# Kernel tuning notes

Measured on AMD Instinct MI355X. Metric: run time of the kernel, lower is better.

## Reference

```python
import jax, jax.numpy as jnp
import numpy as np

N_NODES = 20000
N_EDGES = 640000
C_IN = 128      # num_node_features
K_FOLDS = 8     # num_edge_features
FILTERS = 128


def setup_inputs() -> dict:
    key = jax.random.key(0)
    k1, k2, k3, k4, k5, k6 = jax.random.split(key, 6)
    node_features = jax.random.normal(k1, (N_NODES, C_IN), dtype=jnp.float32)
    edge_features = jax.random.uniform(k2, (K_FOLDS, N_EDGES), dtype=jnp.float32)
    rows = jax.random.randint(k3, (N_EDGES,), 0, N_NODES)
    cols = jax.random.randint(k4, (N_EDGES,), 0, N_NODES)
    indices = jnp.stack([rows, cols], axis=1).astype(jnp.int64)
    # glorot_uniform kernel [K, C_in, filters]
    limit = np.sqrt(6.0 / (C_IN + FILTERS))
    kernel = jax.random.uniform(k5, (K_FOLDS, C_IN, FILTERS), dtype=jnp.float32,
                                minval=-limit, maxval=limit)
    bias = jnp.zeros((FILTERS,), dtype=jnp.float32)
    return {
        "node_features": node_features,
        "edge_features": edge_features,
        "kernel": kernel,
        "bias": bias,
        "indices": indices,
        "out_size": N_NODES,
    }


def reference(node_features, edge_features, kernel, bias, indices, out_size):
    # fold_conv: out[i,f] = sum_{e: row(e)=i} sum_k ef[k,e] * (x[col(e)] @ kernel[k])[f]
    row = indices[:, 0]
    col = indices[:, 1]
    xg = node_features[col]  # [E, C] gathered source-node features
    E = xg.shape[0]
    msgs = jnp.zeros((E, kernel.shape[2]), dtype=node_features.dtype)
    # Loop over the small fixed number of folds (K=8); each iteration is a
    # dense [E,C]x[C,F] matmul scaled by the per-edge fold weight.
    for k in range(kernel.shape[0]):
        msgs = msgs + (xg @ kernel[k]) * edge_features[k][:, None]
    out = jax.ops.segment_sum(msgs, row, num_segments=out_size)  # [out_size, F]
    out = out + bias  # bias_add; activation is None (linear)
    return out
```

## Files before the change

kernel.cpp:

```cpp
#include <hip/hip_runtime.h>
#include <cstddef>
#include <cstdint>

static constexpr int kNodes   = 20000;
static constexpr int kEdges   = 640000;
static constexpr int kCin     = 128;
static constexpr int kFolds   = 8;
static constexpr int kFilters = 128;
static constexpr int kKdim    = kFolds * kCin;
static constexpr int kCap     = 80;

static constexpr int kNBucket = 250;
static constexpr int kRowsPB  = 80;
static constexpr int kCapB    = 3072;
static constexpr int kBin1Blk = 160;

typedef __attribute__((ext_vector_type(8))) short v8s;
typedef __attribute__((ext_vector_type(4))) float v4f;

__device__ __forceinline__ unsigned short f2bf(float f) {
    union { float f; uint32_t u; } v; v.f = f;
    const uint32_t u = v.u;
    return (unsigned short)((u + 0x7fffu + ((u >> 16) & 1u)) >> 16);
}
__device__ __forceinline__ float bf2f(unsigned short s) {
    union { uint32_t u; float f; } v; v.u = ((uint32_t)s) << 16;
    return v.f;
}

__global__ __launch_bounds__(256) void prep_k(
    const int2*  __restrict__ idx2,
    const float* __restrict__ ef,
    const float* __restrict__ x,
    const float* __restrict__ W,
    int* __restrict__ bucketCnt,
    int2* __restrict__ pairs,
    unsigned int* __restrict__ rec,
    unsigned short* __restrict__ xb,
    unsigned short* __restrict__ Wt)
{
    const int b = blockIdx.x;
    const int t = threadIdx.x;
    if (b < 2500) {
        const int e = b * 256 + t;
        const int2 rc = idx2[e];
        union { uint4 q; unsigned int w[4]; unsigned short s[8]; } o;
        #pragma unroll
        for (int k = 0; k < kFolds; ++k)
            o.s[k] = f2bf(ef[(size_t)k * kEdges + e]);
        uint4* recp = (uint4*)(rec + (size_t)e * 8);
        recp[0] = make_uint4((unsigned)rc.y, o.w[0], o.w[1], o.w[2]);
        recp[1] = make_uint4(o.w[3], 0u, 0u, 0u);
    } else if (b < 3750) {
        const int i = (b - 2500) * 2048 + t * 8;
        const float4 a = *(const float4*)(x + i);
        const float4 c = *(const float4*)(x + i + 4);
        union { uint4 q; unsigned short s[8]; } o;
        o.s[0] = f2bf(a.x); o.s[1] = f2bf(a.y); o.s[2] = f2bf(a.z); o.s[3] = f2bf(a.w);
        o.s[4] = f2bf(c.x); o.s[5] = f2bf(c.y); o.s[6] = f2bf(c.z); o.s[7] = f2bf(c.w);
        *(uint4*)(xb + i) = o.q;
    } else if (b < 3814) {
        const int t2 = (b - 3750) * 256 + t;
        const int n  = t2 & 127;
        const int k8 = t2 >> 7;
        union { uint4 q; unsigned short s[8]; } o;
        #pragma unroll
        for (int j = 0; j < 8; ++j)
            o.s[j] = f2bf(W[(size_t)(k8 * 8 + j) * kFilters + n]);
        *(uint4*)(Wt + (size_t)n * kKdim + k8 * 8) = o.q;
    } else {
        __shared__ int hist[kNBucket];
        __shared__ int base[kNBucket];
        const int bb = b - 3814;
        const int e0 = bb * 4096;

        if (t < kNBucket) hist[t] = 0;
        __syncthreads();

        int rowsReg[16];
        #pragma unroll
        for (int i = 0; i < 16; ++i) {
            const int e = e0 + i * 256 + t;
            int row = -1;
            if (e < kEdges) {
                row = idx2[e].x;
                atomicAdd(&hist[row / kRowsPB], 1);
            }
            rowsReg[i] = row;
        }
        __syncthreads();

        if (t < kNBucket) {
            const int h = hist[t];
            base[t] = atomicAdd(&bucketCnt[t], h);
            hist[t] = 0;
        }
        __syncthreads();

        #pragma unroll
        for (int i = 0; i < 16; ++i) {
            const int row = rowsReg[i];
            if (row >= 0) {
                const int e  = e0 + i * 256 + t;
                const int bk = row / kRowsPB;
                const int sl = base[bk] + atomicAdd(&hist[bk], 1);
                if (sl < kCapB)
                    pairs[(size_t)bk * kCapB + sl] = make_int2(row, e);
            }
        }
    }
}

__global__ __launch_bounds__(256) void bin2_k(
    const int2* __restrict__ pairs,
    const int*  __restrict__ bucketCnt,
    int* __restrict__ ebuf,
    int* __restrict__ cnt)
{
    __shared__ int c80[kRowsPB];
    const int b = blockIdx.x;
    const int t = threadIdx.x;

    if (t < kRowsPB) c80[t] = 0;
    __syncthreads();

    int n = bucketCnt[b];
    n = n < kCapB ? n : kCapB;
    const int2* seg = pairs + (size_t)b * kCapB;

    for (int s = t; s < n; s += 256) {
        const int2 p = seg[s];
        const int rl = p.x - b * kRowsPB;
        const int c  = atomicAdd(&c80[rl], 1);
        if (c < kCap) ebuf[p.x * kCap + c] = p.y;
    }
    __syncthreads();

    if (t < kRowsPB) cnt[b * kRowsPB + t] = c80[t];
}

__global__ __launch_bounds__(256) void pull_k(
    const unsigned short* __restrict__ xb,
    const int*  __restrict__ ebuf,
    const unsigned int* __restrict__ rec,
    const int*  __restrict__ cnt,
    unsigned short* __restrict__ S)
{
    __shared__ int   sCol[16][kCap + 4];
    __shared__ float sEf[16][kCap + 4][8];
    __shared__ int   sDeg[16];

    const int t  = threadIdx.x;
    const int n0 = blockIdx.x * 16;

    {
        const int g16 = t >> 4;
        const int s0  = t & 15;
        const int nn  = n0 + g16;
        int dg = cnt[nn];
        dg = dg < kCap ? dg : kCap;
        for (int s = s0; s < dg; s += 16) {
            const int e = ebuf[nn * kCap + s];
            const uint4 q0    = *(const uint4*)(rec + (size_t)e * 8);
            const unsigned w3 = rec[(size_t)e * 8 + 4];
            sCol[g16][s] = (int)q0.x;
            sEf[g16][s][0] = bf2f((unsigned short)(q0.y));
            sEf[g16][s][1] = bf2f((unsigned short)(q0.y >> 16));
            sEf[g16][s][2] = bf2f((unsigned short)(q0.z));
            sEf[g16][s][3] = bf2f((unsigned short)(q0.z >> 16));
            sEf[g16][s][4] = bf2f((unsigned short)(q0.w));
            sEf[g16][s][5] = bf2f((unsigned short)(q0.w >> 16));
            sEf[g16][s][6] = bf2f((unsigned short)(w3));
            sEf[g16][s][7] = bf2f((unsigned short)(w3 >> 16));
        }
        const int dgP = (dg + 3) & ~3;
        for (int s = dg + s0; s < dgP; s += 16) {
            sCol[g16][s] = 0;
            #pragma unroll
            for (int k = 0; k < kFolds; ++k) sEf[g16][s][k] = 0.f;
        }
        if (s0 == 0) sDeg[g16] = dg;
    }
    __syncthreads();

    const int wave = t >> 6;
    const int lane = t & 63;
    const int g    = lane >> 4;
    const int c8   = (lane & 15) * 8;
    const int ln   = wave * 4 + g;
    const int node = n0 + ln;
    const int degP = (sDeg[ln] + 3) & ~3;

    float acc[8][8];
    #pragma unroll
    for (int k = 0; k < 8; ++k)
        #pragma unroll
        for (int j = 0; j < 8; ++j) acc[k][j] = 0.f;

    const unsigned short* xbase = xb + c8;

    auto proc = [&](v8s xv, int i) {
        float xf[8];
        #pragma unroll
        for (int jj = 0; jj < 8; ++jj) xf[jj] = bf2f((unsigned short)xv[jj]);
        const float4 wa = *(const float4*)&sEf[ln][i][0];
        const float4 wc = *(const float4*)&sEf[ln][i][4];
        const float w[8] = {wa.x, wa.y, wa.z, wa.w, wc.x, wc.y, wc.z, wc.w};
        #pragma unroll
        for (int k = 0; k < 8; ++k)
            #pragma unroll
            for (int jj = 0; jj < 8; ++jj)
                acc[k][jj] += w[k] * xf[jj];
    };

    v8s x0 = (v8s)0, x1 = (v8s)0, x2 = (v8s)0, x3 = (v8s)0;
    if (degP > 0) {
        x0 = *(const v8s*)(xbase + (size_t)sCol[ln][0] * kCin);
        x1 = *(const v8s*)(xbase + (size_t)sCol[ln][1] * kCin);
        x2 = *(const v8s*)(xbase + (size_t)sCol[ln][2] * kCin);
        x3 = *(const v8s*)(xbase + (size_t)sCol[ln][3] * kCin);
    }

    for (int i = 0; i < degP; i += 4) {
        const int j = (i + 4 < degP) ? (i + 4) : i;
        const v8s y0 = *(const v8s*)(xbase + (size_t)sCol[ln][j]     * kCin);
        const v8s y1 = *(const v8s*)(xbase + (size_t)sCol[ln][j + 1] * kCin);
        const v8s y2 = *(const v8s*)(xbase + (size_t)sCol[ln][j + 2] * kCin);
        const v8s y3 = *(const v8s*)(xbase + (size_t)sCol[ln][j + 3] * kCin);

        proc(x0, i); proc(x1, i + 1); proc(x2, i + 2); proc(x3, i + 3);

        x0 = y0; x1 = y1; x2 = y2; x3 = y3;
    }

    unsigned short* srow = S + (size_t)node * kKdim + c8;
    #pragma unroll
    for (int k = 0; k < 8; ++k) {
        union { uint4 q; unsigned short s[8]; } o;
        #pragma unroll
        for (int j = 0; j < 8; ++j) o.s[j] = f2bf(acc[k][j]);
        *(uint4*)(srow + k * kCin) = o.q;
    }
}

static constexpr int BM  = 64;
static constexpr int BK  = 64;
static constexpr int SWS = 72;

__global__ __launch_bounds__(256) void gemm_k(
    const unsigned short* __restrict__ S,
    const unsigned short* __restrict__ Wt,
    const float* __restrict__ bias,
    float* __restrict__ out)
{
    __shared__ unsigned short sS[BM * SWS];
    __shared__ unsigned short sWt[kFilters * SWS];

    const int t    = threadIdx.x;
    const int wave = t >> 6;
    const int lane = t & 63;
    const int quad = lane >> 4;
    const int r16  = lane & 15;
    const int m0   = blockIdx.x * BM;

    v4f acc[8];
    #pragma unroll
    for (int i = 0; i < 8; ++i) acc[i] = (v4f){0.f, 0.f, 0.f, 0.f};

    for (int k0 = 0; k0 < kKdim; k0 += BK) {
        {
            const int row = t >> 2;
            const int kc  = (t & 3) * 16;
            const int m   = m0 + row;
            uint4 v0 = make_uint4(0, 0, 0, 0), v1 = make_uint4(0, 0, 0, 0);
            if (m < kNodes) {
                const unsigned short* src = S + (size_t)m * kKdim + k0 + kc;
                v0 = *(const uint4*)(src);
                v1 = *(const uint4*)(src + 8);
            }
            *(uint4*)&sS[row * SWS + kc]     = v0;
            *(uint4*)&sS[row * SWS + kc + 8] = v1;
        }
        {
            const int n    = t >> 1;
            const int half = (t & 1) * 32;
            const unsigned short* src = Wt + (size_t)n * kKdim + k0 + half;
            *(uint4*)&sWt[n * SWS + half]      = *(const uint4*)(src);
            *(uint4*)&sWt[n * SWS + half + 8]  = *(const uint4*)(src + 8);
            *(uint4*)&sWt[n * SWS + half + 16] = *(const uint4*)(src + 16);
            *(uint4*)&sWt[n * SWS + half + 24] = *(const uint4*)(src + 24);
        }
        __syncthreads();

        #pragma unroll
        for (int kk = 0; kk < 2; ++kk) {
            const v8s a = *(const v8s*)&sS[(wave * 16 + r16) * SWS + kk * 32 + quad * 8];
            #pragma unroll
            for (int nt = 0; nt < 8; ++nt) {
                const v8s b = *(const v8s*)&sWt[(nt * 16 + r16) * SWS + kk * 32 + quad * 8];
                acc[nt] = __builtin_amdgcn_mfma_f32_16x16x32_bf16(a, b, acc[nt], 0, 0, 0);
            }
        }
        __syncthreads();
    }

    #pragma unroll
    for (int nt = 0; nt < 8; ++nt) {
        const int n = nt * 16 + r16;
        const float bv = bias[n];
        #pragma unroll
        for (int r = 0; r < 4; ++r) {
            const int m = m0 + wave * 16 + quad * 4 + r;
            if (m < kNodes)
                out[(size_t)m * kFilters + n] = acc[nt][r] + bv;
        }
    }
}

extern "C" void kernel_launch(void* const* d_in, const int* in_sizes, int n_in,
                              void* d_out, int out_size, void* d_ws, size_t ws_size,
                              hipStream_t stream) {
    const float* x    = (const float*)d_in[0];
    const float* ef   = (const float*)d_in[1];
    const float* W    = (const float*)d_in[2];
    const float* bias = (const float*)d_in[3];
    const int2*  idx2 = (const int2*)d_in[4];
    float* out = (float*)d_out;

    char* ws = (char*)d_ws;
    unsigned short* S      = (unsigned short*)(ws);
    int2*           pairs  = (int2*)(ws);
    unsigned int*   rec    = (unsigned int*)(ws + 40960000);
    int*            ebuf   = (int*)(ws + 61440000);
    unsigned short* xb     = (unsigned short*)(ws + 67840000);
    unsigned short* Wt     = (unsigned short*)(ws + 72960000);
    int*            cnt    = (int*)(ws + 73222144);
    int*            bucketCnt = (int*)(ws + 73302144);

    hipMemsetAsync(bucketCnt, 0, kNBucket * sizeof(int), stream);

    prep_k<<<3814 + kBin1Blk, 256, 0, stream>>>(idx2, ef, x, W, bucketCnt,
                                                pairs, rec, xb, Wt);
    bin2_k<<<kNBucket, 256, 0, stream>>>(pairs, bucketCnt, ebuf, cnt);
    pull_k<<<kNodes / 16, 256, 0, stream>>>(xb, ebuf, rec, cnt, S);
    gemm_k<<<(kNodes + BM - 1) / BM, 256, 0, stream>>>(S, Wt, bias, out);
}
```

Measured before the change: 183.6 us.

## Fuse the GEMM into the pull kernel, dropping the S intermediate buffer

After: 192.0 us. 1.05x slower.

```diff
diff --git a/kernel.cpp b/kernel.cpp
--- a/kernel.cpp
+++ b/kernel.cpp
@@ -139,16 +139,23 @@
     if (t < kRowsPB) cnt[b * kRowsPB + t] = c80[t];
 }
 
+static constexpr int kSWS2 = 1048;
+
 __global__ __launch_bounds__(256) void pull_k(
     const unsigned short* __restrict__ xb,
     const int*  __restrict__ ebuf,
     const unsigned int* __restrict__ rec,
     const int*  __restrict__ cnt,
-    unsigned short* __restrict__ S)
+    const unsigned short* __restrict__ Wt,
+    const float* __restrict__ bias,
+    float* __restrict__ out)
 {
-    __shared__ int   sCol[16][kCap + 4];
-    __shared__ float sEf[16][kCap + 4][8];
-    __shared__ int   sDeg[16];
+    __shared__ int sCol[16][kCap + 4];
+    __shared__ int sDeg[16];
+    __shared__ __align__(16) char arena[16 * (kCap + 4) * 8 * 4];
+
+    float (*sEf)[kCap + 4][8] = (float(*)[kCap + 4][8])arena;
+    unsigned short (*sS)[kSWS2] = (unsigned short(*)[kSWS2])arena;
 
     const int t  = threadIdx.x;
     const int n0 = blockIdx.x * 16;
@@ -188,7 +195,6 @@
     const int g    = lane >> 4;
     const int c8   = (lane & 15) * 8;
     const int ln   = wave * 4 + g;
-    const int node = n0 + ln;
     const int degP = (sDeg[ln] + 3) & ~3;
 
     float acc[8][8];
@@ -233,86 +239,43 @@
         x0 = y0; x1 = y1; x2 = y2; x3 = y3;
     }
 
-    unsigned short* srow = S + (size_t)node * kKdim + c8;
+    __syncthreads();
     #pragma unroll
     for (int k = 0; k < 8; ++k) {
         union { uint4 q; unsigned short s[8]; } o;
         #pragma unroll
         for (int j = 0; j < 8; ++j) o.s[j] = f2bf(acc[k][j]);
-        *(uint4*)(srow + k * kCin) = o.q;
-    }
-}
-
-static constexpr int BM  = 64;
-static constexpr int BK  = 64;
-static constexpr int SWS = 72;
-
-__global__ __launch_bounds__(256) void gemm_k(
-    const unsigned short* __restrict__ S,
-    const unsigned short* __restrict__ Wt,
-    const float* __restrict__ bias,
-    float* __restrict__ out)
-{
-    __shared__ unsigned short sS[BM * SWS];
-    __shared__ unsigned short sWt[kFilters * SWS];
-
-    const int t    = threadIdx.x;
-    const int wave = t >> 6;
-    const int lane = t & 63;
+        *(uint4*)&sS[ln][k * kCin + c8] = o.q;
+    }
+    __syncthreads();
+
     const int quad = lane >> 4;
     const int r16  = lane & 15;
-    const int m0   = blockIdx.x * BM;
-
-    v4f acc[8];
+
+    v4f acc2[2];
+    acc2[0] = (v4f){0.f, 0.f, 0.f, 0.f};
+    acc2[1] = (v4f){0.f, 0.f, 0.f, 0.f};
+
+    const unsigned short* wt0 = Wt + (size_t)(wave * 32 + r16) * kKdim;
+    const unsigned short* wt1 = wt0 + (size_t)16 * kKdim;
+
+    #pragma unroll 4
+    for (int kc = 0; kc < kKdim; kc += 32) {
+        const v8s a  = *(const v8s*)&sS[r16][kc + quad * 8];
+        const v8s b0 = *(const v8s*)(wt0 + kc + quad * 8);
+        const v8s b1 = *(const v8s*)(wt1 + kc + quad * 8);
+        acc2[0] = __builtin_amdgcn_mfma_f32_16x16x32_bf16(a, b0, acc2[0], 0, 0, 0);
+        acc2[1] = __builtin_amdgcn_mfma_f32_16x16x32_bf16(a, b1, acc2[1], 0, 0, 0);
+    }
+
     #pragma unroll
-    for (int i = 0; i < 8; ++i) acc[i] = (v4f){0.f, 0.f, 0.f, 0.f};
-
-    for (int k0 = 0; k0 < kKdim; k0 += BK) {
-        {
-            const int row = t >> 2;
-            const int kc  = (t & 3) * 16;
-            const int m   = m0 + row;
-            uint4 v0 = make_uint4(0, 0, 0, 0), v1 = make_uint4(0, 0, 0, 0);
-            if (m < kNodes) {
-                const unsigned short* src = S + (size_t)m * kKdim + k0 + kc;
-                v0 = *(const uint4*)(src);
-                v1 = *(const uint4*)(src + 8);
-            }
-            *(uint4*)&sS[row * SWS + kc]     = v0;
-            *(uint4*)&sS[row * SWS + kc + 8] = v1;
-        }
-        {
-            const int n    = t >> 1;
-            const int half = (t & 1) * 32;
-            const unsigned short* src = Wt + (size_t)n * kKdim + k0 + half;
-            *(uint4*)&sWt[n * SWS + half]      = *(const uint4*)(src);
-            *(uint4*)&sWt[n * SWS + half + 8]  = *(const uint4*)(src + 8);
-            *(uint4*)&sWt[n * SWS + half + 16] = *(const uint4*)(src + 16);
-            *(uint4*)&sWt[n * SWS + half + 24] = *(const uint4*)(src + 24);
-        }
-        __syncthreads();
-
-        #pragma unroll
-        for (int kk = 0; kk < 2; ++kk) {
-            const v8s a = *(const v8s*)&sS[(wave * 16 + r16) * SWS + kk * 32 + quad * 8];
-            #pragma unroll
-            for (int nt = 0; nt < 8; ++nt) {
-                const v8s b = *(const v8s*)&sWt[(nt * 16 + r16) * SWS + kk * 32 + quad * 8];
-                acc[nt] = __builtin_amdgcn_mfma_f32_16x16x32_bf16(a, b, acc[nt], 0, 0, 0);
-            }
-        }
-        __syncthreads();
-    }
-
-    #pragma unroll
-    for (int nt = 0; nt < 8; ++nt) {
-        const int n = nt * 16 + r16;
+    for (int i = 0; i < 2; ++i) {
+        const int n  = (wave * 2 + i) * 16 + r16;
         const float bv = bias[n];
         #pragma unroll
         for (int r = 0; r < 4; ++r) {
-            const int m = m0 + wave * 16 + quad * 4 + r;
-            if (m < kNodes)
-                out[(size_t)m * kFilters + n] = acc[nt][r] + bv;
+            const int m = n0 + quad * 4 + r;
+            out[(size_t)m * kFilters + n] = acc2[i][r] + bv;
         }
     }
 }
@@ -328,7 +291,6 @@
     float* out = (float*)d_out;
 
     char* ws = (char*)d_ws;
-    unsigned short* S      = (unsigned short*)(ws);
     int2*           pairs  = (int2*)(ws);
     unsigned int*   rec    = (unsigned int*)(ws + 40960000);
     int*            ebuf   = (int*)(ws + 61440000);
@@ -342,6 +304,5 @@
     prep_k<<<3814 + kBin1Blk, 256, 0, stream>>>(idx2, ef, x, W, bucketCnt,
                                                 pairs, rec, xb, Wt);
     bin2_k<<<kNBucket, 256, 0, stream>>>(pairs, bucketCnt, ebuf, cnt);
-    pull_k<<<kNodes / 16, 256, 0, stream>>>(xb, ebuf, rec, cnt, S);
-    gemm_k<<<(kNodes + BM - 1) / BM, 256, 0, stream>>>(S, Wt, bias, out);
-}
+    pull_k<<<kNodes / 16, 256, 0, stream>>>(xb, ebuf, rec, cnt, Wt, bias, out);
+}
```
